# Performance work log

Measured on AMD Instinct MI355X. Metric: run time of the kernel, lower is better.

The kernel has to match this reference:

```python
import jax, jax.numpy as jnp
import numpy as np

B, NQ, NV, DIM, HEADS, K = 2, 2048, 2048, 256, 8, 8
HD = DIM // HEADS
HID = 4 * DIM
SCALE = HD ** -0.5
EPS = 1e-5


def setup_inputs() -> dict:
    key = jax.random.key(0)
    ks = jax.random.split(key, 40)
    r = lambda i, s: jax.random.normal(ks[i], s, jnp.float32) * 0.02
    inp = {
        'q': jax.random.normal(ks[0], (B, NQ, DIM), jnp.float32),
        'v': jax.random.normal(ks[1], (B, NV, DIM), jnp.float32),
        'q_pos': jax.random.normal(ks[2], (B, NQ, 3), jnp.float32),
        'v_pos': jax.random.normal(ks[3], (B, NV, 3), jnp.float32),
        'self_knn_index': jax.random.randint(ks[4], (B, NQ, K), 0, NQ, jnp.int32),
        'cross_knn_index': jax.random.randint(ks[5], (B, NQ, K), 0, NV, jnp.int32),
        # LayerNorms (gamma=1, beta=0)
        'norm1_g': jnp.ones(DIM), 'norm1_b': jnp.zeros(DIM),
        'normq_g': jnp.ones(DIM), 'normq_b': jnp.zeros(DIM),
        'normv_g': jnp.ones(DIM), 'normv_b': jnp.zeros(DIM),
        'norm2_g': jnp.ones(DIM), 'norm2_b': jnp.zeros(DIM),
        # self-attention (qkv_bias=False), proj has bias
        'sa_qkv_w': r(6, (DIM, 3 * DIM)),
        'sa_proj_w': r(7, (DIM, DIM)), 'sa_proj_b': jnp.zeros(DIM),
        # cross-attention: q proj and kv proj (no bias), out proj with bias
        'ca_q_w': r(8, (DIM, DIM)),
        'ca_kv_w': r(9, (DIM, 2 * DIM)),
        'ca_proj_w': r(10, (DIM, DIM)), 'ca_proj_b': jnp.zeros(DIM),
        # MLP
        'fc1_w': r(11, (DIM, HID)), 'fc1_b': jnp.zeros(HID),
        'fc2_w': r(12, (HID, DIM)), 'fc2_b': jnp.zeros(DIM),
        # kNN maps
        'knn_w': r(13, (2 * DIM, DIM)), 'knn_b': jnp.zeros(DIM),
        'merge_w': r(14, (2 * DIM, DIM)), 'merge_b': jnp.zeros(DIM),
        'knnx_w': r(15, (2 * DIM, DIM)), 'knnx_b': jnp.zeros(DIM),
        'mergex_w': r(16, (2 * DIM, DIM)), 'mergex_b': jnp.zeros(DIM),
    }
    return inp


def _ln(x, g, b):
    m = x.mean(-1, keepdims=True)
    var = x.var(-1, keepdims=True)
    return (x - m) / jnp.sqrt(var + EPS) * g + b


def _heads(x):  # [B,N,DIM] -> [B,H,N,HD]
    Bx, N, _ = x.shape
    return x.reshape(Bx, N, HEADS, HD).transpose(0, 2, 1, 3)


def _attend(qh, kh, vh, proj_w, proj_b):
    a = jax.nn.softmax(jnp.einsum('bhqd,bhkd->bhqk', qh, kh) * SCALE, axis=-1)
    o = jnp.einsum('bhqk,bhkd->bhqd', a, vh)
    Bx, _, N, _ = o.shape
    o = o.transpose(0, 2, 1, 3).reshape(Bx, N, DIM)
    return o @ proj_w + proj_b


_gather = jax.vmap(lambda pts, idx: pts[idx])  # ([N,D],[Nq,K]) -> [Nq,K,D]


def _knn_feature(qn, vn, idx):  # gather -> diff/cat -> [B,Nq,K,2D]
    local = _gather(vn, idx)                      # [B,Nq,K,D]
    qe = qn[:, :, None, :]                        # [B,Nq,1,D]
    return jnp.concatenate([local - qe, jnp.broadcast_to(qe, local.shape)], -1)


def reference(q, v, q_pos, v_pos, self_knn_index, cross_knn_index,
              norm1_g, norm1_b, normq_g, normq_b, normv_g, normv_b,
              norm2_g, norm2_b, sa_qkv_w, sa_proj_w, sa_proj_b,
              ca_q_w, ca_kv_w, ca_proj_w, ca_proj_b,
              fc1_w, fc1_b, fc2_w, fc2_b,
              knn_w, knn_b, merge_w, merge_b,
              knnx_w, knnx_b, mergex_w, mergex_b):
    # ---- self-attention block with self-kNN branch ----
    nq = _ln(q, norm1_g, norm1_b)
    qkv = nq @ sa_qkv_w
    qh, kh, vh = (_heads(t) for t in jnp.split(qkv, 3, axis=-1))
    sa_out = _attend(qh, kh, vh, sa_proj_w, sa_proj_b)
    f = _knn_feature(nq, nq, self_knn_index)
    knn_out = jax.nn.leaky_relu(f @ knn_w + knn_b, 0.2).max(axis=-2)
    q1 = jnp.concatenate([sa_out, knn_out], -1) @ merge_w + merge_b
    q = q + q1
    # ---- cross-attention block with cross-kNN branch ----
    nq2 = _ln(q, normq_g, normq_b)
    nv = _ln(v, normv_g, normv_b)
    qh = _heads(nq2 @ ca_q_w)
    kh, vh = (_heads(t) for t in jnp.split(nv @ ca_kv_w, 2, axis=-1))
    ca_out = _attend(qh, kh, vh, ca_proj_w, ca_proj_b)
    f = _knn_feature(nq2, nv, cross_knn_index)
    knnx_out = jax.nn.leaky_relu(f @ knnx_w + knnx_b, 0.2).max(axis=-2)
    q2 = jnp.concatenate([ca_out, knnx_out], -1) @ mergex_w + mergex_b
    q = q + q2
    # ---- MLP block ----
    h = _ln(q, norm2_g, norm2_b)
    h = jax.nn.gelu(h @ fc1_w + fc1_b, approximate=False)
    q = q + (h @ fc2_w + fc2_b)
    return q
```

## Files before the change

kernel.cpp:

```cpp
#include <hip/hip_runtime.h>
#include <math.h>

#define NQC   2048
#define NKVC  2048
#define DIMC  256
#define SCALEF 0.17677669529663687f

typedef short bfrag __attribute__((ext_vector_type(8)));
typedef float ffrag __attribute__((ext_vector_type(4)));
typedef unsigned short us8 __attribute__((ext_vector_type(8)));

__device__ __forceinline__ float gelu_exact(float x) {
    return 0.5f * x * (1.0f + erff(x * 0.70710678118654752f));
}
__device__ __forceinline__ unsigned short f2bf(float f) {
    union { float f; unsigned u; } v; v.f = f;
    unsigned r = v.u + 0x7FFFu + ((v.u >> 16) & 1u);
    return (unsigned short)(r >> 16);
}
__device__ __forceinline__ float bf2f(unsigned short u) {
    union { unsigned u; float f; } v; v.u = ((unsigned)u) << 16;
    return v.f;
}

__global__ __launch_bounds__(256) void prep_w(
    const float* __restrict__ qkv, const float* __restrict__ knn,
    const float* __restrict__ proj, const float* __restrict__ merge,
    const float* __restrict__ caq, const float* __restrict__ knnx,
    const float* __restrict__ cakv, const float* __restrict__ projx,
    const float* __restrict__ mergex, const float* __restrict__ fc1,
    const float* __restrict__ fc2, unsigned short* __restrict__ dst)
{
    int e = (blockIdx.x * 256 + threadIdx.x) * 4;
    float v[4];
    float scale = 1.0f;
    if (e < 327680) {
        int n = e >> 8, k = e & 255;
        if (n < 768) {
            const float* s = qkv + (size_t)k * 768 + n;
            #pragma unroll
            for (int i = 0; i < 4; ++i) v[i] = s[(size_t)i * 768];
            if (n < 256) scale = SCALEF;
        } else if (n < 1024) {
            const float* s = knn + (size_t)k * 256 + (n - 768);
            #pragma unroll
            for (int i = 0; i < 4; ++i) v[i] = s[(size_t)i * 256];
        } else {
            const float* s = knn + (size_t)k * 256 + (n - 1024);
            #pragma unroll
            for (int i = 0; i < 4; ++i) v[i] = s[65536 + (size_t)i * 256] - s[(size_t)i * 256];
        }
    } else if (e < 393216) {
        int l = e - 327680, n = l >> 8, k = l & 255;
        const float* s = proj + (size_t)k * 256 + n;
        #pragma unroll
        for (int i = 0; i < 4; ++i) v[i] = s[(size_t)i * 256];
    } else if (e < 524288) {
        int l = e - 393216, n = l >> 9, k = l & 511;
        const float* s = merge + (size_t)k * 256 + n;
        #pragma unroll
        for (int i = 0; i < 4; ++i) v[i] = s[(size_t)i * 256];
    } else if (e < 655360) {
        int l = e - 524288, n = l >> 8, k = l & 255;
        if (n < 256) {
            const float* s = caq + (size_t)k * 256 + n;
            #pragma unroll
            for (int i = 0; i < 4; ++i) v[i] = s[(size_t)i * 256];
            scale = SCALEF;
        } else {
            const float* s = knnx + (size_t)k * 256 + (n - 256);
            #pragma unroll
            for (int i = 0; i < 4; ++i) v[i] = s[65536 + (size_t)i * 256] - s[(size_t)i * 256];
        }
    } else if (e < 851968) {
        int l = e - 655360, n = l >> 8, k = l & 255;
        if (n < 512) {
            const float* s = cakv + (size_t)k * 512 + n;
            #pragma unroll
            for (int i = 0; i < 4; ++i) v[i] = s[(size_t)i * 512];
        } else {
            const float* s = knnx + (size_t)k * 256 + (n - 512);
            #pragma unroll
            for (int i = 0; i < 4; ++i) v[i] = s[(size_t)i * 256];
        }
    } else if (e < 917504) {
        int l = e - 851968, n = l >> 8, k = l & 255;
        const float* s = projx + (size_t)k * 256 + n;
        #pragma unroll
        for (int i = 0; i < 4; ++i) v[i] = s[(size_t)i * 256];
    } else if (e < 1048576) {
        int l = e - 917504, n = l >> 9, k = l & 511;
        const float* s = mergex + (size_t)k * 256 + n;
        #pragma unroll
        for (int i = 0; i < 4; ++i) v[i] = s[(size_t)i * 256];
    } else if (e < 1310720) {
        int l = e - 1048576, n = l >> 8, k = l & 255;
        const float* s = fc1 + (size_t)k * 1024 + n;
        #pragma unroll
        for (int i = 0; i < 4; ++i) v[i] = s[(size_t)i * 1024];
    } else {
        int l = e - 1310720, n = l >> 10, k = l & 1023;
        const float* s = fc2 + (size_t)k * 256 + n;
        #pragma unroll
        for (int i = 0; i < 4; ++i) v[i] = s[(size_t)i * 256];
    }
    ushort4 o;
    o.x = f2bf(v[0] * scale); o.y = f2bf(v[1] * scale);
    o.z = f2bf(v[2] * scale); o.w = f2bf(v[3] * scale);
    *(ushort4*)(dst + e) = o;
}

__global__ __launch_bounds__(256) void ln_b(
    const float* __restrict__ x, const float* __restrict__ g,
    const float* __restrict__ b, unsigned short* __restrict__ y)
{
    int wid = threadIdx.x >> 6, lane = threadIdx.x & 63;
    int row = blockIdx.x * 4 + wid;
    const float* xr = x + (size_t)row * DIMC + lane * 4;
    float4 vv = *(const float4*)xr;
    float s  = vv.x + vv.y + vv.z + vv.w;
    float sq = vv.x*vv.x + vv.y*vv.y + vv.z*vv.z + vv.w*vv.w;
    #pragma unroll
    for (int off = 32; off >= 1; off >>= 1) {
        s  += __shfl_xor(s, off);
        sq += __shfl_xor(sq, off);
    }
    float mean = s * (1.0f/DIMC);
    float var  = sq * (1.0f/DIMC) - mean*mean;
    float inv  = rsqrtf(var + 1e-5f);
    float4 gg = *(const float4*)(g + lane*4);
    float4 bb = *(const float4*)(b + lane*4);
    ushort4 o;
    o.x = f2bf((vv.x - mean) * inv * gg.x + bb.x);
    o.y = f2bf((vv.y - mean) * inv * gg.y + bb.y);
    o.z = f2bf((vv.z - mean) * inv * gg.z + bb.z);
    o.w = f2bf((vv.w - mean) * inv * gg.w + bb.w);
    *(ushort4*)(y + (size_t)row * DIMC + lane * 4) = o;
}

template<int ACT, int RESID, int OUTBF>
__global__ __launch_bounds__(256) void gemm64(
    const unsigned short* __restrict__ A, int lda,
    const unsigned short* __restrict__ Wt,
    const float* __restrict__ bias,
    const float* __restrict__ resid, int ldr,
    void* __restrict__ Cp, int ldc, int Kc)
{
    __shared__ unsigned short Alds[64][72];
    __shared__ unsigned short Wlds[64][72];
    const int tid = threadIdx.x;
    const int wid = tid >> 6, lane = tid & 63;
    const int lm = lane & 15, quad = lane >> 4;
    const int wr = wid >> 1, wc = wid & 1;
    const int row0 = blockIdx.y * 64, col0 = blockIdx.x * 64;
    const int ar = tid >> 2, ac = (tid & 3) * 16;
    const unsigned short* Ag = A  + (size_t)(row0 + ar) * lda + ac;
    const unsigned short* Wg = Wt + (size_t)(col0 + ar) * Kc  + ac;

    us8 a0 = *(const us8*)Ag;
    us8 a1 = *(const us8*)(Ag + 8);
    us8 w0 = *(const us8*)Wg;
    us8 w1 = *(const us8*)(Wg + 8);

    ffrag acc[2][2];
    #pragma unroll
    for (int mi = 0; mi < 2; ++mi)
        #pragma unroll
        for (int ni = 0; ni < 2; ++ni)
            acc[mi][ni] = (ffrag){0.f, 0.f, 0.f, 0.f};

    for (int k0 = 0;;) {
        __syncthreads();
        *(us8*)&Alds[ar][ac]   = a0;
        *(us8*)&Alds[ar][ac+8] = a1;
        *(us8*)&Wlds[ar][ac]   = w0;
        *(us8*)&Wlds[ar][ac+8] = w1;
        __syncthreads();
        k0 += 64;
        if (k0 < Kc) {
            a0 = *(const us8*)(Ag + k0);
            a1 = *(const us8*)(Ag + k0 + 8);
            w0 = *(const us8*)(Wg + k0);
            w1 = *(const us8*)(Wg + k0 + 8);
        }
        #pragma unroll
        for (int kc = 0; kc < 2; ++kc) {
            bfrag af[2], bw[2];
            #pragma unroll
            for (int mi = 0; mi < 2; ++mi)
                af[mi] = *(const bfrag*)&Alds[wr*32 + mi*16 + lm][kc*32 + quad*8];
            #pragma unroll
            for (int ni = 0; ni < 2; ++ni)
                bw[ni] = *(const bfrag*)&Wlds[wc*32 + ni*16 + lm][kc*32 + quad*8];
            #pragma unroll
            for (int mi = 0; mi < 2; ++mi)
                #pragma unroll
                for (int ni = 0; ni < 2; ++ni)
                    acc[mi][ni] = __builtin_amdgcn_mfma_f32_16x16x32_bf16(
                        af[mi], bw[ni], acc[mi][ni], 0, 0, 0);
        }
        if (k0 >= Kc) break;
    }
    #pragma unroll
    for (int mi = 0; mi < 2; ++mi) {
        #pragma unroll
        for (int ni = 0; ni < 2; ++ni) {
            int gr = row0 + wr*32 + mi*16 + quad*4;
            int gc = col0 + wc*32 + ni*16 + lm;
            float bv = bias ? bias[gc] : 0.f;
            #pragma unroll
            for (int r = 0; r < 4; ++r) {
                float o = acc[mi][ni][r] + bv;
                if (ACT == 1) o = gelu_exact(o);
                if (RESID) o += resid[(size_t)(gr + r) * ldr + gc];
                if (OUTBF) ((unsigned short*)Cp)[(size_t)(gr + r) * ldc + gc] = f2bf(o);
                else       ((float*)Cp)[(size_t)(gr + r) * ldc + gc] = o;
            }
        }
    }
}

__global__ __launch_bounds__(256) void attn_part(
    const unsigned short* __restrict__ Qp, int ldq,
    const unsigned short* __restrict__ Kp, int ldk,
    const unsigned short* __restrict__ Vp, int ldv,
    unsigned short* __restrict__ Op, float* __restrict__ Lp)
{
    __shared__ unsigned short Klds[64][40];
    __shared__ unsigned short Vt[32][72];
    __shared__ unsigned short Plds[4][16][72];
    int zc = blockIdx.z, bb = zc >> 1, ck = zc & 1;
    int h = blockIdx.y;
    int hoff = h * 32;
    int tid = threadIdx.x, wid = tid >> 6, lane = tid & 63;
    int lm = lane & 15, quad = lane >> 4;
    size_t qbase  = (size_t)bb * NQC;
    size_t kvbase = (size_t)bb * NKVC;
    int q0 = blockIdx.x * 64 + wid * 16;

    bfrag aq = *(const bfrag*)(Qp + (qbase + q0 + lm) * (size_t)ldq + hoff + quad * 8);

    float l_r[4] = {0.f, 0.f, 0.f, 0.f};
    ffrag oacc[2];
    oacc[0] = (ffrag){0.f, 0.f, 0.f, 0.f};
    oacc[1] = (ffrag){0.f, 0.f, 0.f, 0.f};

    const int kkey = tid >> 2, kd0 = (tid & 3) * 8;
    const int vkey = tid & 63, vd0 = (tid >> 6) * 8;
    const unsigned short* kg0 = Kp + (kvbase + kkey) * (size_t)ldk + hoff + kd0;
    const unsigned short* vg0 = Vp + (kvbase + vkey) * (size_t)ldv + hoff + vd0;

    for (int kt = ck * 16; kt < ck * 16 + 16; ++kt) {
        us8 kv = *(const us8*)(kg0 + (size_t)kt * 64 * ldk);
        us8 vv = *(const us8*)(vg0 + (size_t)kt * 64 * ldv);
        __syncthreads();
        *(us8*)&Klds[kkey][kd0] = kv;
        #pragma unroll
        for (int i = 0; i < 8; ++i) Vt[vd0 + i][vkey] = vv[i];
        __syncthreads();

        ffrag sacc[4];
        #pragma unroll
        for (int t = 0; t < 4; ++t) {
            bfrag bk = *(const bfrag*)&Klds[t*16 + lm][quad * 8];
            sacc[t] = __builtin_amdgcn_mfma_f32_16x16x32_bf16(
                aq, bk, (ffrag){0.f,0.f,0.f,0.f}, 0, 0, 0);
        }

        #pragma unroll
        for (int r = 0; r < 4; ++r) {
            float p0 = __expf(sacc[0][r]), p1 = __expf(sacc[1][r]);
            float p2 = __expf(sacc[2][r]), p3 = __expf(sacc[3][r]);
            l_r[r] += (p0 + p1) + (p2 + p3);
            int row = quad * 4 + r;
            Plds[wid][row][lm +  0] = f2bf(p0);
            Plds[wid][row][lm + 16] = f2bf(p1);
            Plds[wid][row][lm + 32] = f2bf(p2);
            Plds[wid][row][lm + 48] = f2bf(p3);
        }
        asm volatile("s_waitcnt lgkmcnt(0)" ::: "memory");

        #pragma unroll
        for (int kc = 0; kc < 2; ++kc) {
            bfrag ap = *(const bfrag*)&Plds[wid][lm][kc*32 + quad*8];
            #pragma unroll
            for (int nt = 0; nt < 2; ++nt) {
                bfrag bv = *(const bfrag*)&Vt[nt*16 + lm][kc*32 + quad*8];
                oacc[nt] = __builtin_amdgcn_mfma_f32_16x16x32_bf16(
                    ap, bv, oacc[nt], 0, 0, 0);
            }
        }
    }
    #pragma unroll
    for (int nt = 0; nt < 2; ++nt)
        #pragma unroll
        for (int r = 0; r < 4; ++r)
            Op[((size_t)ck * 4096 + qbase + q0 + quad*4 + r) * 256 + hoff + nt*16 + lm]
                = f2bf(oacc[nt][r]);
    #pragma unroll
    for (int r = 0; r < 4; ++r) {
        float l = l_r[r];
        l += __shfl_xor(l, 1);
        l += __shfl_xor(l, 2);
        l += __shfl_xor(l, 4);
        l += __shfl_xor(l, 8);
        if (lm == 0)
            Lp[((size_t)ck * 4096 + qbase + q0 + quad*4 + r) * 8 + h] = l;
    }
}

__global__ __launch_bounds__(256) void attn_comb(
    const unsigned short* __restrict__ Op, const float* __restrict__ Lp,
    unsigned short* __restrict__ dst)
{
    int wid = threadIdx.x >> 6, lane = threadIdx.x & 63;
    int row = blockIdx.x * 4 + wid;
    int c = lane * 4, h = c >> 5;
    ushort4 o0 = *(const ushort4*)(Op + (size_t)row * 256 + c);
    ushort4 o1 = *(const ushort4*)(Op + (size_t)(4096 + row) * 256 + c);
    float inv = 1.0f / (Lp[(size_t)row * 8 + h] + Lp[(size_t)(4096 + row) * 8 + h]);
    ushort4 o;
    o.x = f2bf((bf2f(o0.x) + bf2f(o1.x)) * inv);
    o.y = f2bf((bf2f(o0.y) + bf2f(o1.y)) * inv);
    o.z = f2bf((bf2f(o0.z) + bf2f(o1.z)) * inv);
    o.w = f2bf((bf2f(o0.w) + bf2f(o1.w)) * inv);
    *(ushort4*)(dst + (size_t)row * 256 + c) = o;
}

__global__ __launch_bounds__(256) void gathermax_b(
    const unsigned short* __restrict__ P, int ldp,
    const unsigned short* __restrict__ Base, int ldb,
    const float* __restrict__ bias, const int* __restrict__ idx,
    unsigned short* __restrict__ out, int ldo)
{
    int wid = threadIdx.x >> 6, lane = threadIdx.x & 63;
    int q = blockIdx.x * 4 + wid;
    int b = q >> 11;
    int c = lane * 4;
    ushort4 bu = *(const ushort4*)(Base + (size_t)q * ldb + c);
    float4 bi = *(const float4*)(bias + c);
    float bsx = bf2f(bu.x) + bi.x, bsy = bf2f(bu.y) + bi.y;
    float bsz = bf2f(bu.z) + bi.z, bsw = bf2f(bu.w) + bi.w;
    float4 acc = make_float4(-3e38f, -3e38f, -3e38f, -3e38f);
    const int* ip = idx + (size_t)q * 8;
    #pragma unroll
    for (int k = 0; k < 8; ++k) {
        int j = ip[k];
        ushort4 pu = *(const ushort4*)(P + ((size_t)(b * NKVC + j)) * ldp + c);
        float t;
        t = bsx + bf2f(pu.x); t = t > 0.f ? t : 0.2f * t; acc.x = fmaxf(acc.x, t);
        t = bsy + bf2f(pu.y); t = t > 0.f ? t : 0.2f * t; acc.y = fmaxf(acc.y, t);
        t = bsz + bf2f(pu.z); t = t > 0.f ? t : 0.2f * t; acc.z = fmaxf(acc.z, t);
        t = bsw + bf2f(pu.w); t = t > 0.f ? t : 0.2f * t; acc.w = fmaxf(acc.w, t);
    }
    ushort4 o;
    o.x = f2bf(acc.x); o.y = f2bf(acc.y); o.z = f2bf(acc.z); o.w = f2bf(acc.w);
    *(ushort4*)(out + (size_t)q * ldo + c) = o;
}

extern "C" void kernel_launch(void* const* d_in, const int* in_sizes, int n_in,
                              void* d_out, int out_size, void* d_ws, size_t ws_size,
                              hipStream_t stream) {
    const float* q_in   = (const float*)d_in[0];
    const float* v_in   = (const float*)d_in[1];
    const int*   idx_s  = (const int*)d_in[4];
    const int*   idx_x  = (const int*)d_in[5];
    const float* n1g = (const float*)d_in[6],  *n1b = (const float*)d_in[7];
    const float* nqg = (const float*)d_in[8],  *nqb = (const float*)d_in[9];
    const float* nvg = (const float*)d_in[10], *nvb = (const float*)d_in[11];
    const float* n2g = (const float*)d_in[12], *n2b = (const float*)d_in[13];
    const float* sa_qkv_w  = (const float*)d_in[14];
    const float* sa_proj_w = (const float*)d_in[15];
    const float* sa_proj_b = (const float*)d_in[16];
    const float* ca_q_w    = (const float*)d_in[17];
    const float* ca_kv_w   = (const float*)d_in[18];
    const float* ca_proj_w = (const float*)d_in[19];
    const float* ca_proj_b = (const float*)d_in[20];
    const float* fc1_w = (const float*)d_in[21], *fc1_b = (const float*)d_in[22];
    const float* fc2_w = (const float*)d_in[23], *fc2_b = (const float*)d_in[24];
    const float* knn_w   = (const float*)d_in[25], *knn_b   = (const float*)d_in[26];
    const float* merge_w = (const float*)d_in[27], *merge_b = (const float*)d_in[28];
    const float* knnx_w  = (const float*)d_in[29], *knnx_b  = (const float*)d_in[30];
    const float* mergex_w = (const float*)d_in[31], *mergex_b = (const float*)d_in[32];
    float* out = (float*)d_out;

    unsigned short* A1      = (unsigned short*)d_ws;
    unsigned short* A2      = A1;
    unsigned short* A3      = A1 + (size_t)4096 * 512;
    unsigned short* Hb      = A1;
    unsigned short* attnraw = A1 + (size_t)4096 * 1280;
    unsigned short* CC      = attnraw + (size_t)4096 * 256;
    unsigned short* XB      = CC + (size_t)4096 * 512;
    unsigned short* NVB     = XB + (size_t)4096 * 256;
    unsigned short* WT      = NVB + (size_t)4096 * 256;
    unsigned short* WT1     = WT;
    unsigned short* WTproj  = WT + 327680;
    unsigned short* WTmerge = WT + 393216;
    unsigned short* WT2     = WT + 524288;
    unsigned short* WT3     = WT + 655360;
    unsigned short* WTprojx = WT + 851968;
    unsigned short* WTmergex= WT + 917504;
    unsigned short* WTfc1   = WT + 1048576;
    unsigned short* WTfc2   = WT + 1310720;
    unsigned short* Opart   = WT + 1572864;
    float* Lpart = (float*)(Opart + (size_t)2 * 4096 * 256);

    dim3 blk(256);
    dim3 gAttn(NQC / 64, 8, 4);

    prep_w<<<dim3(1536), blk, 0, stream>>>(sa_qkv_w, knn_w, sa_proj_w, merge_w,
        ca_q_w, knnx_w, ca_kv_w, ca_proj_w, mergex_w, fc1_w, fc2_w, WT);

    ln_b<<<dim3(1024), blk, 0, stream>>>(q_in, n1g, n1b, XB);
    gemm64<0,0,1><<<dim3(20,64), blk, 0, stream>>>(XB, 256, WT1,
        nullptr, nullptr, 0, A1, 1280, 256);
    attn_part<<<gAttn, blk, 0, stream>>>(A1, 1280, A1+256, 1280, A1+512, 1280,
        Opart, Lpart);
    attn_comb<<<dim3(1024), blk, 0, stream>>>(Opart, Lpart, attnraw);
    gathermax_b<<<dim3(1024), blk, 0, stream>>>(A1+768, 1280, A1+1024, 1280,
        knn_b, idx_s, CC+256, 512);
    gemm64<0,0,1><<<dim3(4,64), blk, 0, stream>>>(attnraw, 256, WTproj,
        sa_proj_b, nullptr, 0, CC, 512, 256);
    gemm64<0,1,0><<<dim3(4,64), blk, 0, stream>>>(CC, 512, WTmerge,
        merge_b, q_in, 256, out, 256, 512);

    ln_b<<<dim3(1024), blk, 0, stream>>>(out, nqg, nqb, XB);
    ln_b<<<dim3(1024), blk, 0, stream>>>(v_in, nvg, nvb, NVB);
    gemm64<0,0,1><<<dim3(8,64), blk, 0, stream>>>(XB, 256, WT2,
        nullptr, nullptr, 0, A2, 512, 256);
    gemm64<0,0,1><<<dim3(12,64), blk, 0, stream>>>(NVB, 256, WT3,
        nullptr, nullptr, 0, A3, 768, 256);
    attn_part<<<gAttn, blk, 0, stream>>>(A2, 512, A3, 768, A3+256, 768,
        Opart, Lpart);
    attn_comb<<<dim3(1024), blk, 0, stream>>>(Opart, Lpart, attnraw);
    gathermax_b<<<dim3(1024), blk, 0, stream>>>(A3+512, 768, A2+256, 512,
        knnx_b, idx_x, CC+256, 512);
    gemm64<0,0,1><<<dim3(4,64), blk, 0, stream>>>(attnraw, 256, WTprojx,
        ca_proj_b, nullptr, 0, CC, 512, 256);
    gemm64<0,1,0><<<dim3(4,64), blk, 0, stream>>>(CC, 512, WTmergex,
        mergex_b, out, 256, out, 256, 512);

    ln_b<<<dim3(1024), blk, 0, stream>>>(out, n2g, n2b, XB);
    gemm64<1,0,1><<<dim3(16,64), blk, 0, stream>>>(XB, 256, WTfc1,
        fc1_b, nullptr, 0, Hb, 1024, 256);
    gemm64<0,1,0><<<dim3(4,64), blk, 0, stream>>>(Hb, 1024, WTfc2,
        fc2_b, out, 256, out, 256, 1024);
}
```

Baseline: 277.8 us.

## Fuse attention split-combine into proj GEMM and add 128x128 tiled GEMM

Drops the separate attn_comb kernel by folding the two-split normalisation (sum partial outputs, divide by summed denominators) into the A-tile load of the projection GEMM. This removes one launch and one write-read round trip of the combined attention buffer per attention block. It also adds a 128x128-tile GEMM with a 4x4 MFMA tile per wave for the wide QKV, KV and fc1 projections, which raises operand reuse per block but halves the block count and raises register pressure.

After: 286.2 us. +3.0%, slower.

```diff
diff --git a/kernel.cpp b/kernel.cpp
--- a/kernel.cpp
+++ b/kernel.cpp
@@ -138,6 +138,82 @@
     *(ushort4*)(y + (size_t)row * DIMC + lane * 4) = o;
 }
 
+template<int ACT>
+__global__ __launch_bounds__(256) void gemm128(
+    const unsigned short* __restrict__ A, int lda,
+    const unsigned short* __restrict__ Wt,
+    const float* __restrict__ bias,
+    unsigned short* __restrict__ C, int ldc, int Kc)
+{
+    __shared__ unsigned short Alds[128][40];
+    __shared__ unsigned short Wlds[128][40];
+    const int tid = threadIdx.x;
+    const int wid = tid >> 6, lane = tid & 63;
+    const int lm = lane & 15, quad = lane >> 4;
+    const int wr = wid >> 1, wc = wid & 1;
+    const int row0 = blockIdx.y * 128, col0 = blockIdx.x * 128;
+    const int ar = tid >> 1, ac = (tid & 1) * 16;
+    const unsigned short* Ag = A  + (size_t)(row0 + ar) * lda + ac;
+    const unsigned short* Wg = Wt + (size_t)(col0 + ar) * Kc  + ac;
+
+    us8 a0 = *(const us8*)Ag;
+    us8 a1 = *(const us8*)(Ag + 8);
+    us8 w0 = *(const us8*)Wg;
+    us8 w1 = *(const us8*)(Wg + 8);
+
+    ffrag acc[4][4];
+    #pragma unroll
+    for (int mi = 0; mi < 4; ++mi)
+        #pragma unroll
+        for (int ni = 0; ni < 4; ++ni)
+            acc[mi][ni] = (ffrag){0.f, 0.f, 0.f, 0.f};
+
+    for (int k0 = 0;;) {
+        __syncthreads();
+        *(us8*)&Alds[ar][ac]   = a0;
+        *(us8*)&Alds[ar][ac+8] = a1;
+        *(us8*)&Wlds[ar][ac]   = w0;
+        *(us8*)&Wlds[ar][ac+8] = w1;
+        __syncthreads();
+        k0 += 32;
+        if (k0 < Kc) {
+            a0 = *(const us8*)(Ag + k0);
+            a1 = *(const us8*)(Ag + k0 + 8);
+            w0 = *(const us8*)(Wg + k0);
+            w1 = *(const us8*)(Wg + k0 + 8);
+        }
+        bfrag af[4], bw[4];
+        #pragma unroll
+        for (int mi = 0; mi < 4; ++mi)
+            af[mi] = *(const bfrag*)&Alds[wr*64 + mi*16 + lm][quad*8];
+        #pragma unroll
+        for (int ni = 0; ni < 4; ++ni)
+            bw[ni] = *(const bfrag*)&Wlds[wc*64 + ni*16 + lm][quad*8];
+        #pragma unroll
+        for (int mi = 0; mi < 4; ++mi)
+            #pragma unroll
+            for (int ni = 0; ni < 4; ++ni)
+                acc[mi][ni] = __builtin_amdgcn_mfma_f32_16x16x32_bf16(
+                    af[mi], bw[ni], acc[mi][ni], 0, 0, 0);
+        if (k0 >= Kc) break;
+    }
+    #pragma unroll
+    for (int mi = 0; mi < 4; ++mi) {
+        #pragma unroll
+        for (int ni = 0; ni < 4; ++ni) {
+            int gr = row0 + wr*64 + mi*16 + quad*4;
+            int gc = col0 + wc*64 + ni*16 + lm;
+            float bv = bias ? bias[gc] : 0.f;
+            #pragma unroll
+            for (int r = 0; r < 4; ++r) {
+                float o = acc[mi][ni][r] + bv;
+                if (ACT == 1) o = gelu_exact(o);
+                C[(size_t)(gr + r) * ldc + gc] = f2bf(o);
+            }
+        }
+    }
+}
+
 template<int ACT, int RESID, int OUTBF>
 __global__ __launch_bounds__(256) void gemm64(
     const unsigned short* __restrict__ A, int lda,
@@ -216,6 +292,97 @@
                 if (OUTBF) ((unsigned short*)Cp)[(size_t)(gr + r) * ldc + gc] = f2bf(o);
                 else       ((float*)Cp)[(size_t)(gr + r) * ldc + gc] = o;
             }
+        }
+    }
+}
+
+__global__ __launch_bounds__(256) void gemm64_comb(
+    const unsigned short* __restrict__ Op, const float* __restrict__ Lp,
+    const unsigned short* __restrict__ Wt,
+    const float* __restrict__ bias,
+    unsigned short* __restrict__ C, int ldc)
+{
+    __shared__ unsigned short Alds[64][72];
+    __shared__ unsigned short Wlds[64][72];
+    const int tid = threadIdx.x;
+    const int wid = tid >> 6, lane = tid & 63;
+    const int lm = lane & 15, quad = lane >> 4;
+    const int wr = wid >> 1, wc = wid & 1;
+    const int row0 = blockIdx.y * 64, col0 = blockIdx.x * 64;
+    const int ar = tid >> 2, ac = (tid & 3) * 16;
+    const int grow = row0 + ar;
+    const unsigned short* O0 = Op + (size_t)grow * 256 + ac;
+    const unsigned short* O1 = Op + (size_t)(4096 + grow) * 256 + ac;
+    const float* L0 = Lp + (size_t)grow * 8;
+    const float* L1 = Lp + (size_t)(4096 + grow) * 8;
+    const unsigned short* Wg = Wt + (size_t)(col0 + ar) * 256 + ac;
+
+    us8 o00 = *(const us8*)O0;
+    us8 o01 = *(const us8*)(O0 + 8);
+    us8 o10 = *(const us8*)O1;
+    us8 o11 = *(const us8*)(O1 + 8);
+    float li = 1.0f / (L0[ac >> 5] + L1[ac >> 5]);
+    us8 w0 = *(const us8*)Wg;
+    us8 w1 = *(const us8*)(Wg + 8);
+
+    ffrag acc[2][2];
+    #pragma unroll
+    for (int mi = 0; mi < 2; ++mi)
+        #pragma unroll
+        for (int ni = 0; ni < 2; ++ni)
+            acc[mi][ni] = (ffrag){0.f, 0.f, 0.f, 0.f};
+
+    for (int k0 = 0;;) {
+        us8 ac0, ac1;
+        #pragma unroll
+        for (int i = 0; i < 8; ++i) {
+            ac0[i] = f2bf((bf2f(o00[i]) + bf2f(o10[i])) * li);
+            ac1[i] = f2bf((bf2f(o01[i]) + bf2f(o11[i])) * li);
+        }
+        __syncthreads();
+        *(us8*)&Alds[ar][ac]   = ac0;
+        *(us8*)&Alds[ar][ac+8] = ac1;
+        *(us8*)&Wlds[ar][ac]   = w0;
+        *(us8*)&Wlds[ar][ac+8] = w1;
+        __syncthreads();
+        k0 += 64;
+        if (k0 < 256) {
+            o00 = *(const us8*)(O0 + k0);
+            o01 = *(const us8*)(O0 + k0 + 8);
+            o10 = *(const us8*)(O1 + k0);
+            o11 = *(const us8*)(O1 + k0 + 8);
+            li = 1.0f / (L0[(k0 + ac) >> 5] + L1[(k0 + ac) >> 5]);
+            w0 = *(const us8*)(Wg + k0);
+            w1 = *(const us8*)(Wg + k0 + 8);
+        }
+        #pragma unroll
+        for (int kc = 0; kc < 2; ++kc) {
+            bfrag af[2], bw[2];
+            #pragma unroll
+            for (int mi = 0; mi < 2; ++mi)
+                af[mi] = *(const bfrag*)&Alds[wr*32 + mi*16 + lm][kc*32 + quad*8];
+            #pragma unroll
+            for (int ni = 0; ni < 2; ++ni)
+                bw[ni] = *(const bfrag*)&Wlds[wc*32 + ni*16 + lm][kc*32 + quad*8];
+            #pragma unroll
+            for (int mi = 0; mi < 2; ++mi)
+                #pragma unroll
+                for (int ni = 0; ni < 2; ++ni)
+                    acc[mi][ni] = __builtin_amdgcn_mfma_f32_16x16x32_bf16(
+                        af[mi], bw[ni], acc[mi][ni], 0, 0, 0);
+        }
+        if (k0 >= 256) break;
+    }
+    #pragma unroll
+    for (int mi = 0; mi < 2; ++mi) {
+        #pragma unroll
+        for (int ni = 0; ni < 2; ++ni) {
+            int gr = row0 + wr*32 + mi*16 + quad*4;
+            int gc = col0 + wc*32 + ni*16 + lm;
+            float bv = bias[gc];
+            #pragma unroll
+            for (int r = 0; r < 4; ++r)
+                C[(size_t)(gr + r) * ldc + gc] = f2bf(acc[mi][ni][r] + bv);
         }
     }
 }
@@ -307,24 +474,6 @@
         if (lm == 0)
             Lp[((size_t)ck * 4096 + qbase + q0 + quad*4 + r) * 8 + h] = l;
     }
-}
-
-__global__ __launch_bounds__(256) void attn_comb(
-    const unsigned short* __restrict__ Op, const float* __restrict__ Lp,
-    unsigned short* __restrict__ dst)
-{
-    int wid = threadIdx.x >> 6, lane = threadIdx.x & 63;
-    int row = blockIdx.x * 4 + wid;
-    int c = lane * 4, h = c >> 5;
-    ushort4 o0 = *(const ushort4*)(Op + (size_t)row * 256 + c);
-    ushort4 o1 = *(const ushort4*)(Op + (size_t)(4096 + row) * 256 + c);
-    float inv = 1.0f / (Lp[(size_t)row * 8 + h] + Lp[(size_t)(4096 + row) * 8 + h]);
-    ushort4 o;
-    o.x = f2bf((bf2f(o0.x) + bf2f(o1.x)) * inv);
-    o.y = f2bf((bf2f(o0.y) + bf2f(o1.y)) * inv);
-    o.z = f2bf((bf2f(o0.z) + bf2f(o1.z)) * inv);
-    o.w = f2bf((bf2f(o0.w) + bf2f(o1.w)) * inv);
-    *(ushort4*)(dst + (size_t)row * 256 + c) = o;
 }
 
 __global__ __launch_bounds__(256) void gathermax_b(
@@ -388,8 +537,7 @@
     unsigned short* A2      = A1;
     unsigned short* A3      = A1 + (size_t)4096 * 512;
     unsigned short* Hb      = A1;
-    unsigned short* attnraw = A1 + (size_t)4096 * 1280;
-    unsigned short* CC      = attnraw + (size_t)4096 * 256;
+    unsigned short* CC      = A1 + (size_t)4096 * 1280;
     unsigned short* XB      = CC + (size_t)4096 * 512;
     unsigned short* NVB     = XB + (size_t)4096 * 256;
     unsigned short* WT      = NVB + (size_t)4096 * 256;
@@ -412,15 +560,14 @@
         ca_q_w, knnx_w, ca_kv_w, ca_proj_w, mergex_w, fc1_w, fc2_w, WT);
 
     ln_b<<<dim3(1024), blk, 0, stream>>>(q_in, n1g, n1b, XB);
-    gemm64<0,0,1><<<dim3(20,64), blk, 0, stream>>>(XB, 256, WT1,
-        nullptr, nullptr, 0, A1, 1280, 256);
+    gemm128<0><<<dim3(10,32), blk, 0, stream>>>(XB, 256, WT1,
+        nullptr, A1, 1280, 256);
     attn_part<<<gAttn, blk, 0, stream>>>(A1, 1280, A1+256, 1280, A1+512, 1280,
         Opart, Lpart);
-    attn_comb<<<dim3(1024), blk, 0, stream>>>(Opart, Lpart, attnraw);
     gathermax_b<<<dim3(1024), blk, 0, stream>>>(A1+768, 1280, A1+1024, 1280,
         knn_b, idx_s, CC+256, 512);
-    gemm64<0,0,1><<<dim3(4,64), blk, 0, stream>>>(attnraw, 256, WTproj,
-        sa_proj_b, nullptr, 0, CC, 512, 256);
+    gemm64_comb<<<dim3(4,64), blk, 0, stream>>>(Opart, Lpart, WTproj,
+        sa_proj_b, CC, 512);
     gemm64<0,1,0><<<dim3(4,64), blk, 0, stream>>>(CC, 512, WTmerge,
         merge_b, q_in, 256, out, 256, 512);
 
@@ -428,21 +575,20 @@
     ln_b<<<dim3(1024), blk, 0, stream>>>(v_in, nvg, nvb, NVB);
     gemm64<0,0,1><<<dim3(8,64), blk, 0, stream>>>(XB, 256, WT2,
         nullptr, nullptr, 0, A2, 512, 256);
-    gemm64<0,0,1><<<dim3(12,64), blk, 0, stream>>>(NVB, 256, WT3,
-        nullptr, nullptr, 0, A3, 768, 256);
+    gemm128<0><<<dim3(6,32), blk, 0, stream>>>(NVB, 256, WT3,
+        nullptr, A3, 768, 256);
     attn_part<<<gAttn, blk, 0, stream>>>(A2, 512, A3, 768, A3+256, 768,
         Opart, Lpart);
-    attn_comb<<<dim3(1024), blk, 0, stream>>>(Opart, Lpart, attnraw);
     gathermax_b<<<dim3(1024), blk, 0, stream>>>(A3+512, 768, A2+256, 512,
         knnx_b, idx_x, CC+256, 512);
-    gemm64<0,0,1><<<dim3(4,64), blk, 0, stream>>>(attnraw, 256, WTprojx,
-        ca_proj_b, nullptr, 0, CC, 512, 256);
+    gemm64_comb<<<dim3(4,64), blk, 0, stream>>>(Opart, Lpart, WTprojx,
+        ca_proj_b, CC, 512);
     gemm64<0,1,0><<<dim3(4,64), blk, 0, stream>>>(CC, 512, WTmergex,
         mergex_b, out, 256, out, 256, 512);
 
     ln_b<<<dim3(1024), blk, 0, stream>>>(out, n2g, n2b, XB);
-    gemm64<1,0,1><<<dim3(16,64), blk, 0, stream>>>(XB, 256, WTfc1,
-        fc1_b, nullptr, 0, Hb, 1024, 256);
+    gemm128<1><<<dim3(8,32), blk, 0, stream>>>(XB, 256, WTfc1,
+        fc1_b, Hb, 1024, 256);
     gemm64<0,1,0><<<dim3(4,64), blk, 0, stream>>>(Hb, 1024, WTfc2,
         fc2_b, out, 256, out, 256, 1024);
 }
```

## Fold attention out-projection into merge weights and fuse combine into merge GEMM

Applied to the files above, without the earlier changes.

Precomputes proj_w·merge_w (and the folded bias) on device, so the attention out-projection GEMM is removed for both the self and cross blocks. The merge GEMM now reads the two partial attention outputs and their row sums directly, normalising them while loading the A tile, which removes the attn_comb kernel and the intermediate buffer. The two back-to-back LayerNorms for q and v are merged into a single launch. The trade is extra per-call weight-folding kernels and rounding the folded product to bf16, which changes numerics slightly.

Measured after the change: 294.1 us. 1.06x slower.

```diff
diff --git a/kernel.cpp b/kernel.cpp
--- a/kernel.cpp
+++ b/kernel.cpp
@@ -108,6 +108,65 @@
     o.x = f2bf(v[0] * scale); o.y = f2bf(v[1] * scale);
     o.z = f2bf(v[2] * scale); o.w = f2bf(v[3] * scale);
     *(ushort4*)(dst + e) = o;
+}
+
+__global__ __launch_bounds__(256) void fold_w(
+    const float* __restrict__ proj, const float* __restrict__ merge,
+    const float* __restrict__ projx, const float* __restrict__ mergex,
+    unsigned short* __restrict__ dst0, unsigned short* __restrict__ dst1)
+{
+    const float* A = blockIdx.z ? projx : proj;
+    const float* B = blockIdx.z ? mergex : merge;
+    unsigned short* D = blockIdx.z ? dst1 : dst0;
+    __shared__ float As[16][64];
+    __shared__ float Bs[16][64];
+    int tid = threadIdx.x;
+    int tx = tid & 15, ty = tid >> 4;
+    int row0 = blockIdx.y * 64, col0 = blockIdx.x * 64;
+    int arow = tid >> 2, acol = (tid & 3) * 4;
+    int brow = tid >> 4, bcol = (tid & 15) * 4;
+    float acc[4][4] = {};
+    for (int j0 = 0; j0 < 256; j0 += 16) {
+        __syncthreads();
+        float4 av = *(const float4*)(A + (size_t)(row0 + arow) * 256 + j0 + acol);
+        float4 bv = *(const float4*)(B + (size_t)(j0 + brow) * 256 + col0 + bcol);
+        As[acol+0][arow] = av.x; As[acol+1][arow] = av.y;
+        As[acol+2][arow] = av.z; As[acol+3][arow] = av.w;
+        *(float4*)&Bs[brow][bcol] = bv;
+        __syncthreads();
+        #pragma unroll
+        for (int j = 0; j < 16; ++j) {
+            float4 a4 = *(const float4*)&As[j][ty*4];
+            float4 b4 = *(const float4*)&Bs[j][tx*4];
+            float ar[4] = {a4.x, a4.y, a4.z, a4.w};
+            float br[4] = {b4.x, b4.y, b4.z, b4.w};
+            #pragma unroll
+            for (int ii = 0; ii < 4; ++ii)
+                #pragma unroll
+                for (int jj = 0; jj < 4; ++jj)
+                    acc[ii][jj] = fmaf(ar[ii], br[jj], acc[ii][jj]);
+        }
+    }
+    #pragma unroll
+    for (int ii = 0; ii < 4; ++ii)
+        #pragma unroll
+        for (int jj = 0; jj < 4; ++jj)
+            D[(size_t)(col0 + tx*4 + jj) * 512 + row0 + ty*4 + ii] = f2bf(acc[ii][jj]);
+}
+
+__global__ __launch_bounds__(256) void fold_bias(
+    const float* __restrict__ pb, const float* __restrict__ mw,
+    const float* __restrict__ mb,
+    const float* __restrict__ pbx, const float* __restrict__ mwx,
+    const float* __restrict__ mbx, float* __restrict__ bn)
+{
+    int z = blockIdx.x, n = threadIdx.x;
+    const float* PB = z ? pbx : pb;
+    const float* MW = z ? mwx : mw;
+    const float* MB = z ? mbx : mb;
+    float s = MB[n];
+    for (int k = 0; k < 256; ++k) s = fmaf(PB[k], MW[(size_t)k * 256 + n], s);
+    bn[z * 256 + n] = s;
 }
 
 __global__ __launch_bounds__(256) void ln_b(
@@ -138,6 +197,39 @@
     *(ushort4*)(y + (size_t)row * DIMC + lane * 4) = o;
 }
 
+__global__ __launch_bounds__(256) void ln2_b(
+    const float* __restrict__ x1, const float* __restrict__ g1,
+    const float* __restrict__ b1, unsigned short* __restrict__ y1,
+    const float* __restrict__ x2, const float* __restrict__ g2,
+    const float* __restrict__ b2, unsigned short* __restrict__ y2)
+{
+    int wid = threadIdx.x >> 6, lane = threadIdx.x & 63;
+    int blk = blockIdx.x;
+    const float* x; const float* g; const float* b; unsigned short* y; int row;
+    if (blk < 1024) { x = x1; g = g1; b = b1; y = y1; row = blk * 4 + wid; }
+    else            { x = x2; g = g2; b = b2; y = y2; row = (blk - 1024) * 4 + wid; }
+    const float* xr = x + (size_t)row * DIMC + lane * 4;
+    float4 vv = *(const float4*)xr;
+    float s  = vv.x + vv.y + vv.z + vv.w;
+    float sq = vv.x*vv.x + vv.y*vv.y + vv.z*vv.z + vv.w*vv.w;
+    #pragma unroll
+    for (int off = 32; off >= 1; off >>= 1) {
+        s  += __shfl_xor(s, off);
+        sq += __shfl_xor(sq, off);
+    }
+    float mean = s * (1.0f/DIMC);
+    float var  = sq * (1.0f/DIMC) - mean*mean;
+    float inv  = rsqrtf(var + 1e-5f);
+    float4 gg = *(const float4*)(g + lane*4);
+    float4 bb = *(const float4*)(b + lane*4);
+    ushort4 o;
+    o.x = f2bf((vv.x - mean) * inv * gg.x + bb.x);
+    o.y = f2bf((vv.y - mean) * inv * gg.y + bb.y);
+    o.z = f2bf((vv.z - mean) * inv * gg.z + bb.z);
+    o.w = f2bf((vv.w - mean) * inv * gg.w + bb.w);
+    *(ushort4*)(y + (size_t)row * DIMC + lane * 4) = o;
+}
+
 template<int ACT, int RESID, int OUTBF>
 __global__ __launch_bounds__(256) void gemm64(
     const unsigned short* __restrict__ A, int lda,
@@ -215,6 +307,106 @@
                 if (RESID) o += resid[(size_t)(gr + r) * ldr + gc];
                 if (OUTBF) ((unsigned short*)Cp)[(size_t)(gr + r) * ldc + gc] = f2bf(o);
                 else       ((float*)Cp)[(size_t)(gr + r) * ldc + gc] = o;
+            }
+        }
+    }
+}
+
+__global__ __launch_bounds__(256) void gemm64_mc(
+    const unsigned short* __restrict__ Op, const float* __restrict__ Lp,
+    const unsigned short* __restrict__ Kn,
+    const unsigned short* __restrict__ Wt,
+    const float* __restrict__ biasN,
+    const float* __restrict__ resid,
+    float* __restrict__ Cp)
+{
+    __shared__ unsigned short Alds[64][72];
+    __shared__ unsigned short Wlds[64][72];
+    const int tid = threadIdx.x;
+    const int wid = tid >> 6, lane = tid & 63;
+    const int lm = lane & 15, quad = lane >> 4;
+    const int wr = wid >> 1, wc = wid & 1;
+    const int row0 = blockIdx.y * 64, col0 = blockIdx.x * 64;
+    const int ar = tid >> 2, ac = (tid & 3) * 16;
+    const int grow = row0 + ar;
+    const unsigned short* O0 = Op + (size_t)grow * 256;
+    const unsigned short* O1 = Op + (size_t)(4096 + grow) * 256;
+    const float* L0 = Lp + (size_t)grow * 8;
+    const float* L1 = Lp + (size_t)(4096 + grow) * 8;
+    const unsigned short* Kr = Kn + (size_t)grow * 256;
+    const unsigned short* Wg = Wt + (size_t)(col0 + ar) * 512;
+
+    us8 a0, a1, w0, w1;
+    auto load_a = [&](int k0, us8& x0, us8& x1) {
+        if (k0 < 256) {
+            us8 o00 = *(const us8*)(O0 + k0 + ac);
+            us8 o01 = *(const us8*)(O0 + k0 + ac + 8);
+            us8 o10 = *(const us8*)(O1 + k0 + ac);
+            us8 o11 = *(const us8*)(O1 + k0 + ac + 8);
+            float li = 1.0f / (L0[(k0 + ac) >> 5] + L1[(k0 + ac) >> 5]);
+            #pragma unroll
+            for (int i = 0; i < 8; ++i) {
+                x0[i] = f2bf((bf2f(o00[i]) + bf2f(o10[i])) * li);
+                x1[i] = f2bf((bf2f(o01[i]) + bf2f(o11[i])) * li);
+            }
+        } else {
+            x0 = *(const us8*)(Kr + k0 - 256 + ac);
+            x1 = *(const us8*)(Kr + k0 - 256 + ac + 8);
+        }
+    };
+    load_a(0, a0, a1);
+    w0 = *(const us8*)(Wg + ac);
+    w1 = *(const us8*)(Wg + ac + 8);
+
+    ffrag acc[2][2];
+    #pragma unroll
+    for (int mi = 0; mi < 2; ++mi)
+        #pragma unroll
+        for (int ni = 0; ni < 2; ++ni)
+            acc[mi][ni] = (ffrag){0.f, 0.f, 0.f, 0.f};
+
+    for (int k0 = 0;;) {
+        __syncthreads();
+        *(us8*)&Alds[ar][ac]   = a0;
+        *(us8*)&Alds[ar][ac+8] = a1;
+        *(us8*)&Wlds[ar][ac]   = w0;
+        *(us8*)&Wlds[ar][ac+8] = w1;
+        __syncthreads();
+        k0 += 64;
+        if (k0 < 512) {
+            load_a(k0, a0, a1);
+            w0 = *(const us8*)(Wg + k0 + ac);
+            w1 = *(const us8*)(Wg + k0 + ac + 8);
+        }
+        #pragma unroll
+        for (int kc = 0; kc < 2; ++kc) {
+            bfrag af[2], bw[2];
+            #pragma unroll
+            for (int mi = 0; mi < 2; ++mi)
+                af[mi] = *(const bfrag*)&Alds[wr*32 + mi*16 + lm][kc*32 + quad*8];
+            #pragma unroll
+            for (int ni = 0; ni < 2; ++ni)
+                bw[ni] = *(const bfrag*)&Wlds[wc*32 + ni*16 + lm][kc*32 + quad*8];
+            #pragma unroll
+            for (int mi = 0; mi < 2; ++mi)
+                #pragma unroll
+                for (int ni = 0; ni < 2; ++ni)
+                    acc[mi][ni] = __builtin_amdgcn_mfma_f32_16x16x32_bf16(
+                        af[mi], bw[ni], acc[mi][ni], 0, 0, 0);
+        }
+        if (k0 >= 512) break;
+    }
+    #pragma unroll
+    for (int mi = 0; mi < 2; ++mi) {
+        #pragma unroll
+        for (int ni = 0; ni < 2; ++ni) {
+            int gr = row0 + wr*32 + mi*16 + quad*4;
+            int gc = col0 + wc*32 + ni*16 + lm;
+            float bv = biasN[gc];
+            #pragma unroll
+            for (int r = 0; r < 4; ++r) {
+                float o = acc[mi][ni][r] + bv + resid[(size_t)(gr + r) * 256 + gc];
+                Cp[(size_t)(gr + r) * 256 + gc] = o;
             }
         }
     }
@@ -307,24 +499,6 @@
         if (lm == 0)
             Lp[((size_t)ck * 4096 + qbase + q0 + quad*4 + r) * 8 + h] = l;
     }
-}
-
-__global__ __launch_bounds__(256) void attn_comb(
-    const unsigned short* __restrict__ Op, const float* __restrict__ Lp,
-    unsigned short* __restrict__ dst)
-{
-    int wid = threadIdx.x >> 6, lane = threadIdx.x & 63;
-    int row = blockIdx.x * 4 + wid;
-    int c = lane * 4, h = c >> 5;
-    ushort4 o0 = *(const ushort4*)(Op + (size_t)row * 256 + c);
-    ushort4 o1 = *(const ushort4*)(Op + (size_t)(4096 + row) * 256 + c);
-    float inv = 1.0f / (Lp[(size_t)row * 8 + h] + Lp[(size_t)(4096 + row) * 8 + h]);
-    ushort4 o;
-    o.x = f2bf((bf2f(o0.x) + bf2f(o1.x)) * inv);
-    o.y = f2bf((bf2f(o0.y) + bf2f(o1.y)) * inv);
-    o.z = f2bf((bf2f(o0.z) + bf2f(o1.z)) * inv);
-    o.w = f2bf((bf2f(o0.w) + bf2f(o1.w)) * inv);
-    *(ushort4*)(dst + (size_t)row * 256 + c) = o;
 }
 
 __global__ __launch_bounds__(256) void gathermax_b(
@@ -388,57 +562,53 @@
     unsigned short* A2      = A1;
     unsigned short* A3      = A1 + (size_t)4096 * 512;
     unsigned short* Hb      = A1;
-    unsigned short* attnraw = A1 + (size_t)4096 * 1280;
-    unsigned short* CC      = attnraw + (size_t)4096 * 256;
-    unsigned short* XB      = CC + (size_t)4096 * 512;
+    unsigned short* KN      = A1 + (size_t)4096 * 1280;
+    unsigned short* XB      = KN + (size_t)4096 * 256;
     unsigned short* NVB     = XB + (size_t)4096 * 256;
     unsigned short* WT      = NVB + (size_t)4096 * 256;
     unsigned short* WT1     = WT;
-    unsigned short* WTproj  = WT + 327680;
     unsigned short* WTmerge = WT + 393216;
     unsigned short* WT2     = WT + 524288;
     unsigned short* WT3     = WT + 655360;
-    unsigned short* WTprojx = WT + 851968;
     unsigned short* WTmergex= WT + 917504;
     unsigned short* WTfc1   = WT + 1048576;
     unsigned short* WTfc2   = WT + 1310720;
     unsigned short* Opart   = WT + 1572864;
     float* Lpart = (float*)(Opart + (size_t)2 * 4096 * 256);
+    float* biasN = Lpart + (size_t)2 * 4096 * 8;
 
     dim3 blk(256);
     dim3 gAttn(NQC / 64, 8, 4);
 
     prep_w<<<dim3(1536), blk, 0, stream>>>(sa_qkv_w, knn_w, sa_proj_w, merge_w,
         ca_q_w, knnx_w, ca_kv_w, ca_proj_w, mergex_w, fc1_w, fc2_w, WT);
+    fold_w<<<dim3(4,4,2), blk, 0, stream>>>(sa_proj_w, merge_w, ca_proj_w,
+        mergex_w, WTmerge, WTmergex);
+    fold_bias<<<dim3(2), blk, 0, stream>>>(sa_proj_b, merge_w, merge_b,
+        ca_proj_b, mergex_w, mergex_b, biasN);
 
     ln_b<<<dim3(1024), blk, 0, stream>>>(q_in, n1g, n1b, XB);
     gemm64<0,0,1><<<dim3(20,64), blk, 0, stream>>>(XB, 256, WT1,
         nullptr, nullptr, 0, A1, 1280, 256);
     attn_part<<<gAttn, blk, 0, stream>>>(A1, 1280, A1+256, 1280, A1+512, 1280,
         Opart, Lpart);
-    attn_comb<<<dim3(1024), blk, 0, stream>>>(Opart, Lpart, attnraw);
     gathermax_b<<<dim3(1024), blk, 0, stream>>>(A1+768, 1280, A1+1024, 1280,
-        knn_b, idx_s, CC+256, 512);
-    gemm64<0,0,1><<<dim3(4,64), blk, 0, stream>>>(attnraw, 256, WTproj,
-        sa_proj_b, nullptr, 0, CC, 512, 256);
-    gemm64<0,1,0><<<dim3(4,64), blk, 0, stream>>>(CC, 512, WTmerge,
-        merge_b, q_in, 256, out, 256, 512);
-
-    ln_b<<<dim3(1024), blk, 0, stream>>>(out, nqg, nqb, XB);
-    ln_b<<<dim3(1024), blk, 0, stream>>>(v_in, nvg, nvb, NVB);
+        knn_b, idx_s, KN, 256);
+    gemm64_mc<<<dim3(4,64), blk, 0, stream>>>(Opart, Lpart, KN, WTmerge,
+        biasN, q_in, out);
+
+    ln2_b<<<dim3(2048), blk, 0, stream>>>(out, nqg, nqb, XB,
+        v_in, nvg, nvb, NVB);
     gemm64<0,0,1><<<dim3(8,64), blk, 0, stream>>>(XB, 256, WT2,
         nullptr, nullptr, 0, A2, 512, 256);
     gemm64<0,0,1><<<dim3(12,64), blk, 0, stream>>>(NVB, 256, WT3,
         nullptr, nullptr, 0, A3, 768, 256);
     attn_part<<<gAttn, blk, 0, stream>>>(A2, 512, A3, 768, A3+256, 768,
         Opart, Lpart);
-    attn_comb<<<dim3(1024), blk, 0, stream>>>(Opart, Lpart, attnraw);
     gathermax_b<<<dim3(1024), blk, 0, stream>>>(A3+512, 768, A2+256, 512,
-        knnx_b, idx_x, CC+256, 512);
-    gemm64<0,0,1><<<dim3(4,64), blk, 0, stream>>>(attnraw, 256, WTprojx,
-        ca_proj_b, nullptr, 0, CC, 512, 256);
-    gemm64<0,1,0><<<dim3(4,64), blk, 0, stream>>>(CC, 512, WTmergex,
-        mergex_b, out, 256, out, 256, 512);
+        knnx_b, idx_x, KN, 256);
+    gemm64_mc<<<dim3(4,64), blk, 0, stream>>>(Opart, Lpart, KN, WTmergex,
+        biasN + 256, out, out);
 
     ln_b<<<dim3(1024), blk, 0, stream>>>(out, n2g, n2b, XB);
     gemm64<1,0,1><<<dim3(16,64), blk, 0, stream>>>(XB, 256, WTfc1,
```
